# Kernel tuning notes

Measured on AMD Instinct MI355X. Metric: run time of the kernel, lower is better.

The kernel has to match this reference:

```python
import jax, jax.numpy as jnp
import numpy as np


def setup_inputs() -> dict:
    key = jax.random.key(0)
    k1, k2, k3, k4 = jax.random.split(key, 4)
    B, Cin, Cout, H, W = 4, 256, 256, 96, 96
    x = jax.random.normal(k1, (B, Cin, H, W), dtype=jnp.float32)
    offset = jax.random.normal(k2, (B, 18, H, W), dtype=jnp.float32)
    mask = jax.random.uniform(k3, (B, 9, H, W), dtype=jnp.float32)
    weight = jax.random.normal(k4, (Cout, Cin, 3, 3), dtype=jnp.float32) * 0.05
    gamma = jnp.ones((Cout,), dtype=jnp.float32)
    beta = jnp.zeros((Cout,), dtype=jnp.float32)
    return {"x": x, "offset": offset, "mask": mask, "weight": weight, "gamma": gamma, "beta": beta}


def reference(x, offset, mask, weight, gamma, beta):
    # Modulated deformable conv v2 (3x3, stride 1, pad 1, no bias) + GroupNorm(8) + ReLU
    B, C, H, W = x.shape
    O = weight.shape[0]
    K = 9
    xh = jnp.transpose(x, (0, 2, 3, 1))  # [B,H,W,C]
    ky, kx = jnp.meshgrid(jnp.arange(3), jnp.arange(3), indexing="ij")
    ky = ky.reshape(1, K, 1, 1).astype(x.dtype)
    kx = kx.reshape(1, K, 1, 1).astype(x.dtype)
    off = offset.reshape(B, K, 2, H, W)  # (dy, dx) per kernel tap, row-major taps
    gy = jnp.arange(H, dtype=x.dtype).reshape(1, 1, H, 1)
    gx = jnp.arange(W, dtype=x.dtype).reshape(1, 1, 1, W)
    py = gy + ky - 1.0 + off[:, :, 0]  # [B,K,H,W] sampling y
    px = gx + kx - 1.0 + off[:, :, 1]  # [B,K,H,W] sampling x
    y0 = jnp.floor(py)
    x0 = jnp.floor(px)
    wy = py - y0
    wx = px - x0
    y0i = y0.astype(jnp.int32)
    x0i = x0.astype(jnp.int32)
    bidx = jnp.arange(B).reshape(B, 1, 1, 1)

    def gather(yi, xi):
        valid = ((yi >= 0) & (yi < H) & (xi >= 0) & (xi < W)).astype(x.dtype)
        v = xh[bidx, jnp.clip(yi, 0, H - 1), jnp.clip(xi, 0, W - 1)]  # [B,K,H,W,C]
        return v * valid[..., None]

    val = (gather(y0i, x0i) * ((1 - wy) * (1 - wx))[..., None]
           + gather(y0i, x0i + 1) * ((1 - wy) * wx)[..., None]
           + gather(y0i + 1, x0i) * (wy * (1 - wx))[..., None]
           + gather(y0i + 1, x0i + 1) * (wy * wx)[..., None])
    val = val * mask[..., None]  # modulation, [B,K,H,W,C]
    out = jnp.einsum("bkhwc,ock->bohw", val, weight.reshape(O, C, K))
    # GroupNorm with 8 groups, eps=1e-5 (affine)
    G = 8
    og = out.reshape(B, G, O // G, H, W)
    mu = og.mean(axis=(2, 3, 4), keepdims=True)
    var = og.var(axis=(2, 3, 4), keepdims=True)
    og = (og - mu) * jax.lax.rsqrt(var + 1e-5)
    out = og.reshape(B, O, H, W) * gamma.reshape(1, O, 1, 1) + beta.reshape(1, O, 1, 1)
    return jax.nn.relu(out)
```

## Files before the change

kernel.cpp:

```cpp
#include <hip/hip_runtime.h>
#include <hip/hip_bf16.h>
#include <stdint.h>

typedef __attribute__((ext_vector_type(4))) float f32x4;
typedef __attribute__((ext_vector_type(8))) short s16x8;
typedef __attribute__((ext_vector_type(4))) unsigned int u32x4;
typedef unsigned short u16;
typedef unsigned int u32;

#define B_ 4
#define C_ 256
#define O_ 256
#define H_ 96
#define W_ 96
#define HW_ (H_*W_)
#define M_ (B_*HW_)

static __device__ __forceinline__ float asf(u32 u){
    union { u32 u; float f; } x; x.u = u; return x.f;
}
static __device__ __forceinline__ u16 f2bf(float f){
    union { float f; u32 u; } x; x.f = f;
    u32 u = x.u;
    u32 r = (u + 0x7fffu + ((u >> 16) & 1u)) >> 16;
    return (u16)r;
}
static __device__ __forceinline__ u32 blerp_pack(u32 q00, u32 q01, u32 q10, u32 q11,
                                                 float w00, float w01, float w10, float w11)
{
    float f0 = asf(q00 << 16) * w00 + asf(q01 << 16) * w01
             + asf(q10 << 16) * w10 + asf(q11 << 16) * w11;
    float f1 = asf(q00) * w00 + asf(q01) * w01 + asf(q10) * w10 + asf(q11) * w11;
    float2 fp; fp.x = f0; fp.y = f1;
    __hip_bfloat162 hb = __float22bfloat162_rn(fp);
    union { __hip_bfloat162 h; u32 u; } cv; cv.h = hb;
    return cv.u;
}

struct TapCtx {
    float w00, w01, w10, w11;
    const u16 *r00, *r01, *r10, *r11;
};

static __device__ __forceinline__ TapCtx tap_setup(
    int tap, int b, int h, int w, int hw,
    const float* __restrict__ off, const float* __restrict__ msk,
    const u16* __restrict__ xT)
{
    TapCtx t;
    float dy = off[(size_t)(b * 18 + 2 * tap) * HW_ + hw];
    float dx = off[(size_t)(b * 18 + 2 * tap + 1) * HW_ + hw];
    float mk = msk[(size_t)(b * 9 + tap) * HW_ + hw];
    float py = (float)(h + tap / 3 - 1) + dy;
    float px = (float)(w + tap % 3 - 1) + dx;
    float fy = floorf(py), fx = floorf(px);
    float wy = py - fy, wx = px - fx;
    int y0 = (int)fy, x0 = (int)fx;
    int y1 = y0 + 1, x1 = x0 + 1;
    float w00 = (1.f - wy) * (1.f - wx) * mk;
    float w01 = (1.f - wy) * wx * mk;
    float w10 = wy * (1.f - wx) * mk;
    float w11 = wy * wx * mk;
    if (y0 < 0 || y0 >= H_) { w00 = 0.f; w01 = 0.f; }
    if (y1 < 0 || y1 >= H_) { w10 = 0.f; w11 = 0.f; }
    if (x0 < 0 || x0 >= W_) { w00 = 0.f; w10 = 0.f; }
    if (x1 < 0 || x1 >= W_) { w01 = 0.f; w11 = 0.f; }
    int cy0 = min(max(y0, 0), H_ - 1), cy1 = min(max(y1, 0), H_ - 1);
    int cx0 = min(max(x0, 0), W_ - 1), cx1 = min(max(x1, 0), W_ - 1);
    size_t rb = (size_t)b * HW_ * C_;
    t.r00 = xT + rb + ((size_t)cy0 * W_ + cx0) * C_;
    t.r01 = xT + rb + ((size_t)cy0 * W_ + cx1) * C_;
    t.r10 = xT + rb + ((size_t)cy1 * W_ + cx0) * C_;
    t.r11 = xT + rb + ((size_t)cy1 * W_ + cx1) * C_;
    t.w00 = w00; t.w01 = w01; t.w10 = w10; t.w11 = w11;
    return t;
}

__global__ __launch_bounds__(256) void transpose_x(const float* __restrict__ x,
                                                   u16* __restrict__ xT)
{
    __shared__ float t[32][33];
    int tid = threadIdx.x;
    int tx = tid & 31, ty = tid >> 5;
    int bi = blockIdx.x;
    int w0 = (bi % 3) * 32;
    int c0 = ((bi / 3) % 8) * 32;
    int bh = bi / 24;
    int b = bh / H_, h = bh - b * H_;
    #pragma unroll
    for (int r = 0; r < 4; ++r){
        int c = c0 + ty + r * 8;
        t[ty + r * 8][tx] = x[(size_t)(b * C_ + c) * HW_ + h * W_ + w0 + tx];
    }
    __syncthreads();
    #pragma unroll
    for (int r = 0; r < 4; ++r){
        int w = w0 + ty + r * 8;
        xT[((size_t)(b * H_ + h) * W_ + w) * C_ + c0 + tx] = f2bf(t[tx][ty + r * 8]);
    }
}

__global__ __launch_bounds__(256) void pack_w(const float* __restrict__ wt,
                                              u16* __restrict__ w3)
{
    int n = blockIdx.x * 256 + threadIdx.x;
    int o = n / 2304;
    int rem = n - o * 2304;
    int c = rem / 9;
    int tap = rem - c * 9;
    int kidx = tap * 256 + c;
    w3[(size_t)(kidx >> 3) * 2048 + o * 8 + (kidx & 7)] = f2bf(wt[n]);
}

__global__ __launch_bounds__(512, 4) void dcn_main(
    const float* __restrict__ off, const float* __restrict__ msk,
    const u16* __restrict__ xT, const u16* __restrict__ w3,
    float* __restrict__ convOut, float* __restrict__ stats)
{
    __shared__ u16 At[64 * 256];
    int tid = threadIdx.x;
    int lane = tid & 63;
    int wv = tid >> 6;
    int l15 = lane & 15;
    int g = lane >> 4;

    int bid = blockIdx.x;
    int tile = (bid & 7) * 72 + (bid >> 3);
    int b = tile / 144;
    int t = tile - b * 144;
    int ty_ = t / 12, tx_ = t - ty_ * 12;
    int py0 = ty_ * 8, px0 = tx_ * 8;

    f32x4 acc[4][2];
    #pragma unroll
    for (int i = 0; i < 4; ++i)
        #pragma unroll
        for (int q = 0; q < 2; ++q)
            acc[i][q] = (f32x4){0.f, 0.f, 0.f, 0.f};

    int p = tid >> 3;
    int k = tid & 7;
    int h = py0 + (p >> 3);
    int w = px0 + (p & 7);
    int hw = h * W_ + w;

    for (int tap = 0; tap < 9; ++tap){
        __syncthreads();
        TapCtx tp = tap_setup(tap, b, h, w, hw, off, msk, xT);
        #pragma unroll
        for (int i = 0; i < 4; ++i){
            int ck = k + i * 8;
            int c = ck * 8;
            u32x4 q00 = *(const u32x4*)(tp.r00 + c);
            u32x4 q01 = *(const u32x4*)(tp.r01 + c);
            u32x4 q10 = *(const u32x4*)(tp.r10 + c);
            u32x4 q11 = *(const u32x4*)(tp.r11 + c);
            u32x4 outv;
            #pragma unroll
            for (int j = 0; j < 4; ++j)
                outv[j] = blerp_pack(q00[j], q01[j], q10[j], q11[j],
                                     tp.w00, tp.w01, tp.w10, tp.w11);
            u32 boff = (u32)(p * 512) + (u32)((ck ^ (p & 15)) << 4);
            *(u32x4*)((char*)At + boff) = outv;
        }
        __syncthreads();
        __builtin_amdgcn_s_setprio(1);
        #pragma unroll
        for (int step = 0; step < 8; ++step){
            int ck = step * 4 + g;
            s16x8 a[4];
            #pragma unroll
            for (int i = 0; i < 4; ++i){
                int r = i * 16 + l15;
                u32 boff = (u32)(r * 512) + (u32)((ck ^ (r & 15)) << 4);
                a[i] = *(const s16x8*)((const char*)At + boff);
            }
            const u16* wrow = w3 + (size_t)(tap * 32 + step * 4 + g) * 2048
                            + (size_t)(wv * 32 + l15) * 8;
            s16x8 b0 = *(const s16x8*)(wrow);
            s16x8 b1 = *(const s16x8*)(wrow + 128);
            #pragma unroll
            for (int i = 0; i < 4; ++i){
                acc[i][0] = __builtin_amdgcn_mfma_f32_16x16x32_bf16(a[i], b0, acc[i][0], 0, 0, 0);
                acc[i][1] = __builtin_amdgcn_mfma_f32_16x16x32_bf16(a[i], b1, acc[i][1], 0, 0, 0);
            }
        }
        __builtin_amdgcn_s_setprio(0);
    }

    float s0 = 0.f, s20 = 0.f;
    size_t mbase = (size_t)b * HW_;
    #pragma unroll
    for (int i = 0; i < 4; ++i){
        #pragma unroll
        for (int q = 0; q < 2; ++q){
            int oc = wv * 32 + q * 16 + l15;
            #pragma unroll
            for (int j = 0; j < 4; ++j){
                float v = acc[i][q][j];
                int pp = i * 16 + g * 4 + j;
                int mr_hw = (py0 + (pp >> 3)) * W_ + px0 + (pp & 7);
                convOut[(mbase + mr_hw) * 256 + oc] = v;
                s0 += v; s20 += v * v;
            }
        }
    }
    #pragma unroll
    for (int d = 32; d; d >>= 1){
        s0  += __shfl_xor(s0, d, 64);
        s20 += __shfl_xor(s20, d, 64);
    }
    if (lane == 0){
        atomicAdd(&stats[(b * 8 + wv) * 2 + 0], s0);
        atomicAdd(&stats[(b * 8 + wv) * 2 + 1], s20);
    }
}

__global__ __launch_bounds__(256) void gn_final(
    const float* __restrict__ convOut, const float* __restrict__ stats,
    const float* __restrict__ gamma, const float* __restrict__ beta,
    float* __restrict__ out)
{
    __shared__ float t[64][257];
    int tid = threadIdx.x;
    int m0 = blockIdx.x * 64;
    int b = m0 / HW_;
    const f32x4* src = (const f32x4*)(convOut + (size_t)m0 * 256);
    #pragma unroll
    for (int it = 0; it < 16; ++it){
        int idx = it * 256 + tid;
        int r = idx >> 6;
        int c4 = idx & 63;
        f32x4 v = src[(size_t)r * 64 + c4];
        t[r][c4 * 4 + 0] = v[0];
        t[r][c4 * 4 + 1] = v[1];
        t[r][c4 * 4 + 2] = v[2];
        t[r][c4 * 4 + 3] = v[3];
    }
    __syncthreads();
    int lanem = tid & 63;
    int hw = (m0 - b * HW_) + lanem;
    float* dst = out + (size_t)b * O_ * HW_ + hw;
    const float invN = 1.f / 294912.f;
    #pragma unroll 8
    for (int it = 0; it < 64; ++it){
        int o = it * 4 + (tid >> 6);
        int gidx = (b * 8 + (o >> 5)) * 2;
        float sm = stats[gidx + 0];
        float sq = stats[gidx + 1];
        float mu = sm * invN;
        float var = sq * invN - mu * mu;
        float inv = rsqrtf(var + 1e-5f);
        float sc = gamma[o] * inv;
        float sh = beta[o] - mu * sc;
        float v = t[lanem][o];
        dst[(size_t)o * HW_] = fmaxf(v * sc + sh, 0.f);
    }
}

extern "C" void kernel_launch(void* const* d_in, const int* in_sizes, int n_in,
                              void* d_out, int out_size, void* d_ws, size_t ws_size,
                              hipStream_t stream)
{
    const float* x     = (const float*)d_in[0];
    const float* off   = (const float*)d_in[1];
    const float* msk   = (const float*)d_in[2];
    const float* wt    = (const float*)d_in[3];
    const float* gamma = (const float*)d_in[4];
    const float* beta  = (const float*)d_in[5];
    float* out = (float*)d_out;

    char* ws = (char*)d_ws;
    u16*   xT      = (u16*)ws;
    u16*   w3      = (u16*)(ws + 18874368);
    float* convOut = (float*)(ws + 20054016);
    float* stats   = (float*)(ws + 57802752);

    hipMemsetAsync(stats, 0, 256, stream);
    hipLaunchKernelGGL(transpose_x, dim3(9216), dim3(256), 0, stream, x, xT);
    hipLaunchKernelGGL(pack_w,      dim3(2304), dim3(256), 0, stream, wt, w3);
    hipLaunchKernelGGL(dcn_main,    dim3(576),  dim3(512), 0, stream,
                       off, msk, xT, w3, convOut, stats);
    hipLaunchKernelGGL(gn_final,    dim3(576),  dim3(256), 0, stream,
                       convOut, stats, gamma, beta, out);
}
```

Baseline: 183.1 us.

## Double-buffer the sampled tile in LDS and overlap next-tap gather with MFMA

Makes the LDS A-tile double-buffered and software-pipelines the tap loop. The bilinear gather loads for tap+1 are issued before the MFMA steps on the current tap, and the interpolated values are written to the other buffer in two halves between the two MFMA halves. This hides global gather latency behind matrix math and cuts the barriers to one per tap. In exchange it doubles LDS use to 64KB per block, which may limit occupancy under launch_bounds(512,4), and it raises register pressure from the prefetched values.

After: 183.8 us. No clear change (+0.4%).

```diff
diff --git a/kernel.cpp b/kernel.cpp
--- a/kernel.cpp
+++ b/kernel.cpp
@@ -117,7 +117,7 @@
     const u16* __restrict__ xT, const u16* __restrict__ w3,
     float* __restrict__ convOut, float* __restrict__ stats)
 {
-    __shared__ u16 At[64 * 256];
+    __shared__ u16 At[2][64 * 256];
     int tid = threadIdx.x;
     int lane = tid & 63;
     int wv = tid >> 6;
@@ -144,9 +144,8 @@
     int w = px0 + (p & 7);
     int hw = h * W_ + w;
 
-    for (int tap = 0; tap < 9; ++tap){
-        __syncthreads();
-        TapCtx tp = tap_setup(tap, b, h, w, hw, off, msk, xT);
+    {
+        TapCtx tp = tap_setup(0, b, h, w, hw, off, msk, xT);
         #pragma unroll
         for (int i = 0; i < 4; ++i){
             int ck = k + i * 8;
@@ -161,19 +160,40 @@
                 outv[j] = blerp_pack(q00[j], q01[j], q10[j], q11[j],
                                      tp.w00, tp.w01, tp.w10, tp.w11);
             u32 boff = (u32)(p * 512) + (u32)((ck ^ (p & 15)) << 4);
-            *(u32x4*)((char*)At + boff) = outv;
-        }
-        __syncthreads();
+            *(u32x4*)((char*)&At[0][0] + boff) = outv;
+        }
+    }
+    __syncthreads();
+
+    int cur = 0;
+    for (int tap = 0; tap < 9; ++tap){
+        bool pre = (tap < 8);
+        TapCtx tn;
+        u32x4 s00[2], s01[2], s10[2], s11[2];
+        if (pre){
+            tn = tap_setup(tap + 1, b, h, w, hw, off, msk, xT);
+            #pragma unroll
+            for (int i = 0; i < 2; ++i){
+                int c = (k + i * 8) * 8;
+                s00[i] = *(const u32x4*)(tn.r00 + c);
+                s01[i] = *(const u32x4*)(tn.r01 + c);
+                s10[i] = *(const u32x4*)(tn.r10 + c);
+                s11[i] = *(const u32x4*)(tn.r11 + c);
+            }
+        }
+        const char* Ac = (const char*)&At[cur][0];
+        char* An = (char*)&At[cur ^ 1][0];
+
         __builtin_amdgcn_s_setprio(1);
         #pragma unroll
-        for (int step = 0; step < 8; ++step){
+        for (int step = 0; step < 4; ++step){
             int ck = step * 4 + g;
             s16x8 a[4];
             #pragma unroll
             for (int i = 0; i < 4; ++i){
                 int r = i * 16 + l15;
                 u32 boff = (u32)(r * 512) + (u32)((ck ^ (r & 15)) << 4);
-                a[i] = *(const s16x8*)((const char*)At + boff);
+                a[i] = *(const s16x8*)(Ac + boff);
             }
             const u16* wrow = w3 + (size_t)(tap * 32 + step * 4 + g) * 2048
                             + (size_t)(wv * 32 + l15) * 8;
@@ -186,6 +206,67 @@
             }
         }
         __builtin_amdgcn_s_setprio(0);
+
+        if (pre){
+            #pragma unroll
+            for (int i = 0; i < 2; ++i){
+                int ck = k + i * 8;
+                u32x4 outv;
+                #pragma unroll
+                for (int j = 0; j < 4; ++j)
+                    outv[j] = blerp_pack(s00[i][j], s01[i][j], s10[i][j], s11[i][j],
+                                         tn.w00, tn.w01, tn.w10, tn.w11);
+                u32 boff = (u32)(p * 512) + (u32)((ck ^ (p & 15)) << 4);
+                *(u32x4*)(An + boff) = outv;
+            }
+            #pragma unroll
+            for (int i = 0; i < 2; ++i){
+                int c = (k + 16 + i * 8) * 8;
+                s00[i] = *(const u32x4*)(tn.r00 + c);
+                s01[i] = *(const u32x4*)(tn.r01 + c);
+                s10[i] = *(const u32x4*)(tn.r10 + c);
+                s11[i] = *(const u32x4*)(tn.r11 + c);
+            }
+        }
+
+        __builtin_amdgcn_s_setprio(1);
+        #pragma unroll
+        for (int step = 4; step < 8; ++step){
+            int ck = step * 4 + g;
+            s16x8 a[4];
+            #pragma unroll
+            for (int i = 0; i < 4; ++i){
+                int r = i * 16 + l15;
+                u32 boff = (u32)(r * 512) + (u32)((ck ^ (r & 15)) << 4);
+                a[i] = *(const s16x8*)(Ac + boff);
+            }
+            const u16* wrow = w3 + (size_t)(tap * 32 + step * 4 + g) * 2048
+                            + (size_t)(wv * 32 + l15) * 8;
+            s16x8 b0 = *(const s16x8*)(wrow);
+            s16x8 b1 = *(const s16x8*)(wrow + 128);
+            #pragma unroll
+            for (int i = 0; i < 4; ++i){
+                acc[i][0] = __builtin_amdgcn_mfma_f32_16x16x32_bf16(a[i], b0, acc[i][0], 0, 0, 0);
+                acc[i][1] = __builtin_amdgcn_mfma_f32_16x16x32_bf16(a[i], b1, acc[i][1], 0, 0, 0);
+            }
+        }
+        __builtin_amdgcn_s_setprio(0);
+
+        if (pre){
+            #pragma unroll
+            for (int i = 0; i < 2; ++i){
+                int ck = k + 16 + i * 8;
+                u32x4 outv;
+                #pragma unroll
+                for (int j = 0; j < 4; ++j)
+                    outv[j] = blerp_pack(s00[i][j], s01[i][j], s10[i][j], s11[i][j],
+                                         tn.w00, tn.w01, tn.w10, tn.w11);
+                u32 boff = (u32)(p * 512) + (u32)((ck ^ (p & 15)) << 4);
+                *(u32x4*)(An + boff) = outv;
+            }
+        }
+        __syncthreads();
+        cur ^= 1;
     }
 
     float s0 = 0.f, s20 = 0.f;
```

## Stage 16x16 halo of input in LDS and prefetch next tap blend

Applied to the files above, without the earlier changes.

Each block now loads a 16x16 spatial halo (half of the channels at a time) of the transposed input into shared memory and reads bilinear corners from LDS when the sampling point falls inside the halo. Points outside fall back to global loads. The bilinear blend for the next tap is computed while the MFMAs for the current tap run, and offset and mask values are prefetched one tap ahead. The kernel splits channels into two passes and drops the occupancy hint in the launch bounds. LDS use grows to about 80KB and an extra barrier is added per tap.

New measurement: 225.2 us. +23.0%, slower.

```diff
diff --git a/kernel.cpp b/kernel.cpp
--- a/kernel.cpp
+++ b/kernel.cpp
@@ -37,20 +37,16 @@
     return cv.u;
 }
 
-struct TapCtx {
+struct QC {
     float w00, w01, w10, w11;
-    const u16 *r00, *r01, *r10, *r11;
+    int y0, x0, r00, fast;
 };
 
-static __device__ __forceinline__ TapCtx tap_setup(
-    int tap, int b, int h, int w, int hw,
-    const float* __restrict__ off, const float* __restrict__ msk,
-    const u16* __restrict__ xT)
-{
-    TapCtx t;
-    float dy = off[(size_t)(b * 18 + 2 * tap) * HW_ + hw];
-    float dx = off[(size_t)(b * 18 + 2 * tap + 1) * HW_ + hw];
-    float mk = msk[(size_t)(b * 9 + tap) * HW_ + hw];
+static __device__ __forceinline__ QC qc_make(int tap, int h, int w,
+                                             float dy, float dx, float mk,
+                                             int hy0, int hx0)
+{
+    QC t;
     float py = (float)(h + tap / 3 - 1) + dy;
     float px = (float)(w + tap % 3 - 1) + dx;
     float fy = floorf(py), fx = floorf(px);
@@ -65,15 +61,51 @@
     if (y1 < 0 || y1 >= H_) { w10 = 0.f; w11 = 0.f; }
     if (x0 < 0 || x0 >= W_) { w00 = 0.f; w10 = 0.f; }
     if (x1 < 0 || x1 >= W_) { w01 = 0.f; w11 = 0.f; }
-    int cy0 = min(max(y0, 0), H_ - 1), cy1 = min(max(y1, 0), H_ - 1);
-    int cx0 = min(max(x0, 0), W_ - 1), cx1 = min(max(x1, 0), W_ - 1);
-    size_t rb = (size_t)b * HW_ * C_;
-    t.r00 = xT + rb + ((size_t)cy0 * W_ + cx0) * C_;
-    t.r01 = xT + rb + ((size_t)cy0 * W_ + cx1) * C_;
-    t.r10 = xT + rb + ((size_t)cy1 * W_ + cx0) * C_;
-    t.r11 = xT + rb + ((size_t)cy1 * W_ + cx1) * C_;
     t.w00 = w00; t.w01 = w01; t.w10 = w10; t.w11 = w11;
+    t.y0 = y0; t.x0 = x0;
+    t.fast = (y0 >= hy0) && (y0 <= hy0 + 14) && (x0 >= hx0) && (x0 <= hx0 + 14);
+    t.r00 = (y0 - hy0) * 16 + (x0 - hx0);
     return t;
+}
+
+static __device__ __forceinline__ void qblend(const QC& c, int k, int cH,
+                                              const u16* Hl, size_t rbimg,
+                                              const u16* __restrict__ xT,
+                                              u32x4 ov[2])
+{
+    const char* Hb = (const char*)Hl;
+    const u16 *b00 = nullptr, *b01 = nullptr, *b10 = nullptr, *b11 = nullptr;
+    if (!c.fast){
+        int cy0 = min(max(c.y0, 0), H_ - 1), cy1 = min(max(c.y0 + 1, 0), H_ - 1);
+        int cx0 = min(max(c.x0, 0), W_ - 1), cx1 = min(max(c.x0 + 1, 0), W_ - 1);
+        const u16* base = xT + rbimg + cH * 128;
+        b00 = base + ((size_t)cy0 * W_ + cx0) * C_;
+        b01 = base + ((size_t)cy0 * W_ + cx1) * C_;
+        b10 = base + ((size_t)cy1 * W_ + cx0) * C_;
+        b11 = base + ((size_t)cy1 * W_ + cx1) * C_;
+    }
+    int r00 = c.r00, r01 = c.r00 + 1, r10 = c.r00 + 16, r11 = c.r00 + 17;
+    #pragma unroll
+    for (int i = 0; i < 2; ++i){
+        int ck = k + 8 * i;
+        u32x4 q00, q01, q10, q11;
+        if (c.fast){
+            q00 = *(const u32x4*)(Hb + r00 * 256 + ((ck ^ (r00 & 15)) << 4));
+            q01 = *(const u32x4*)(Hb + r01 * 256 + ((ck ^ (r01 & 15)) << 4));
+            q10 = *(const u32x4*)(Hb + r10 * 256 + ((ck ^ (r10 & 15)) << 4));
+            q11 = *(const u32x4*)(Hb + r11 * 256 + ((ck ^ (r11 & 15)) << 4));
+        } else {
+            int cc = ck * 8;
+            q00 = *(const u32x4*)(b00 + cc);
+            q01 = *(const u32x4*)(b01 + cc);
+            q10 = *(const u32x4*)(b10 + cc);
+            q11 = *(const u32x4*)(b11 + cc);
+        }
+        #pragma unroll
+        for (int j = 0; j < 4; ++j)
+            ov[i][j] = blerp_pack(q00[j], q01[j], q10[j], q11[j],
+                                  c.w00, c.w01, c.w10, c.w11);
+    }
 }
 
 __global__ __launch_bounds__(256) void transpose_x(const float* __restrict__ x,
@@ -112,12 +144,14 @@
     w3[(size_t)(kidx >> 3) * 2048 + o * 8 + (kidx & 7)] = f2bf(wt[n]);
 }
 
-__global__ __launch_bounds__(512, 4) void dcn_main(
+__global__ __launch_bounds__(512) void dcn_main(
     const float* __restrict__ off, const float* __restrict__ msk,
     const u16* __restrict__ xT, const u16* __restrict__ w3,
     float* __restrict__ convOut, float* __restrict__ stats)
 {
-    __shared__ u16 At[64 * 256];
+    __shared__ u16 Hl[256 * 128];
+    __shared__ u16 At[64 * 128];
+
     int tid = threadIdx.x;
     int lane = tid & 63;
     int wv = tid >> 6;
@@ -143,49 +177,75 @@
     int h = py0 + (p >> 3);
     int w = px0 + (p & 7);
     int hw = h * W_ + w;
-
-    for (int tap = 0; tap < 9; ++tap){
-        __syncthreads();
-        TapCtx tp = tap_setup(tap, b, h, w, hw, off, msk, xT);
+    size_t offb = (size_t)b * 18 * HW_ + hw;
+    size_t mskb = (size_t)b * 9 * HW_ + hw;
+    int hy0 = py0 - 4, hx0 = px0 - 4;
+    size_t rbimg = (size_t)b * HW_ * C_;
+
+    for (int cH = 0; cH < 2; ++cH){
+        float cdy = off[offb];
+        float cdx = off[offb + HW_];
+        float cmk = msk[mskb];
+        float ndy = off[offb + 2 * HW_];
+        float ndx = off[offb + 3 * HW_];
+        float nmk = msk[mskb + HW_];
         #pragma unroll
-        for (int i = 0; i < 4; ++i){
-            int ck = k + i * 8;
-            int c = ck * 8;
-            u32x4 q00 = *(const u32x4*)(tp.r00 + c);
-            u32x4 q01 = *(const u32x4*)(tp.r01 + c);
-            u32x4 q10 = *(const u32x4*)(tp.r10 + c);
-            u32x4 q11 = *(const u32x4*)(tp.r11 + c);
-            u32x4 outv;
-            #pragma unroll
-            for (int j = 0; j < 4; ++j)
-                outv[j] = blerp_pack(q00[j], q01[j], q10[j], q11[j],
-                                     tp.w00, tp.w01, tp.w10, tp.w11);
-            u32 boff = (u32)(p * 512) + (u32)((ck ^ (p & 15)) << 4);
-            *(u32x4*)((char*)At + boff) = outv;
+        for (int it = 0; it < 8; ++it){
+            int u = it * 512 + tid;
+            int row = u >> 4, ck = u & 15;
+            int gy = min(max(hy0 + (row >> 4), 0), H_ - 1);
+            int gx = min(max(hx0 + (row & 15), 0), W_ - 1);
+            u32x4 v = *(const u32x4*)(xT + rbimg + ((size_t)gy * W_ + gx) * C_
+                                      + cH * 128 + ck * 8);
+            *(u32x4*)((char*)Hl + row * 256 + ((ck ^ (row & 15)) << 4)) = v;
         }
         __syncthreads();
-        __builtin_amdgcn_s_setprio(1);
-        #pragma unroll
-        for (int step = 0; step < 8; ++step){
-            int ck = step * 4 + g;
-            s16x8 a[4];
+
+        QC c = qc_make(0, h, w, cdy, cdx, cmk, hy0, hx0);
+        u32x4 ov[2];
+        qblend(c, k, cH, Hl, rbimg, xT, ov);
+
+        for (int tap = 0; tap < 9; ++tap){
             #pragma unroll
-            for (int i = 0; i < 4; ++i){
-                int r = i * 16 + l15;
-                u32 boff = (u32)(r * 512) + (u32)((ck ^ (r & 15)) << 4);
-                a[i] = *(const s16x8*)((const char*)At + boff);
+            for (int i = 0; i < 2; ++i){
+                int ck = k + 8 * i;
+                *(u32x4*)((char*)At + p * 256 + ((ck ^ (p & 15)) << 4)) = ov[i];
             }
-            const u16* wrow = w3 + (size_t)(tap * 32 + step * 4 + g) * 2048
-                            + (size_t)(wv * 32 + l15) * 8;
-            s16x8 b0 = *(const s16x8*)(wrow);
-            s16x8 b1 = *(const s16x8*)(wrow + 128);
+            __syncthreads();
+
+            if (tap < 8){
+                c = qc_make(tap + 1, h, w, ndy, ndx, nmk, hy0, hx0);
+                qblend(c, k, cH, Hl, rbimg, xT, ov);
+                if (tap < 7){
+                    ndy = off[offb + (size_t)(2 * tap + 4) * HW_];
+                    ndx = off[offb + (size_t)(2 * tap + 5) * HW_];
+                    nmk = msk[mskb + (size_t)(tap + 2) * HW_];
+                }
+            }
+            __builtin_amdgcn_s_setprio(1);
             #pragma unroll
-            for (int i = 0; i < 4; ++i){
-                acc[i][0] = __builtin_amdgcn_mfma_f32_16x16x32_bf16(a[i], b0, acc[i][0], 0, 0, 0);
-                acc[i][1] = __builtin_amdgcn_mfma_f32_16x16x32_bf16(a[i], b1, acc[i][1], 0, 0, 0);
+            for (int s = 0; s < 4; ++s){
+                int ck = s * 4 + g;
+                s16x8 a[4];
+                #pragma unroll
+                for (int i = 0; i < 4; ++i){
+                    int r = i * 16 + l15;
+                    a[i] = *(const s16x8*)((const char*)At + r * 256
+                                           + ((ck ^ (r & 15)) << 4));
+                }
+                const u16* wrow = w3 + (size_t)(tap * 32 + cH * 16 + s * 4 + g) * 2048
+                                + (size_t)(wv * 32 + l15) * 8;
+                s16x8 b0 = *(const s16x8*)(wrow);
+                s16x8 b1 = *(const s16x8*)(wrow + 128);
+                #pragma unroll
+                for (int i = 0; i < 4; ++i){
+                    acc[i][0] = __builtin_amdgcn_mfma_f32_16x16x32_bf16(a[i], b0, acc[i][0], 0, 0, 0);
+                    acc[i][1] = __builtin_amdgcn_mfma_f32_16x16x32_bf16(a[i], b1, acc[i][1], 0, 0, 0);
+                }
             }
+            __builtin_amdgcn_s_setprio(0);
+            __syncthreads();
         }
-        __builtin_amdgcn_s_setprio(0);
     }
 
     float s0 = 0.f, s20 = 0.f;
```

## Double-buffer the sampled A tile and overlap next-tap gather with MFMA

Applied to the files above, without the earlier changes.

Doubles the shared-memory A tile and software-pipelines the tap loop. While the MFMAs for the current tap run, the bilinear gather, interpolation and LDS store for the next tap are interleaved in four chunks. This leaves one barrier per tap and lets gather latency hide behind matrix work. It also switches the gather addresses from 64-bit pointers to 32-bit offsets. The cost is twice the LDS (64KB per block) and more live registers, which may reduce occupancy under the 512x4 launch bound.

Measured after the change: 171.2 us. 6.5% less time.

```diff
diff --git a/kernel.cpp b/kernel.cpp
--- a/kernel.cpp
+++ b/kernel.cpp
@@ -39,13 +39,12 @@
 
 struct TapCtx {
     float w00, w01, w10, w11;
-    const u16 *r00, *r01, *r10, *r11;
+    u32 o00, o01, o10, o11;
 };
 
 static __device__ __forceinline__ TapCtx tap_setup(
     int tap, int b, int h, int w, int hw,
-    const float* __restrict__ off, const float* __restrict__ msk,
-    const u16* __restrict__ xT)
+    const float* __restrict__ off, const float* __restrict__ msk)
 {
     TapCtx t;
     float dy = off[(size_t)(b * 18 + 2 * tap) * HW_ + hw];
@@ -67,11 +66,11 @@
     if (x1 < 0 || x1 >= W_) { w01 = 0.f; w11 = 0.f; }
     int cy0 = min(max(y0, 0), H_ - 1), cy1 = min(max(y1, 0), H_ - 1);
     int cx0 = min(max(x0, 0), W_ - 1), cx1 = min(max(x1, 0), W_ - 1);
-    size_t rb = (size_t)b * HW_ * C_;
-    t.r00 = xT + rb + ((size_t)cy0 * W_ + cx0) * C_;
-    t.r01 = xT + rb + ((size_t)cy0 * W_ + cx1) * C_;
-    t.r10 = xT + rb + ((size_t)cy1 * W_ + cx0) * C_;
-    t.r11 = xT + rb + ((size_t)cy1 * W_ + cx1) * C_;
+    u32 rb = (u32)b * (u32)(HW_ * C_);
+    t.o00 = rb + ((u32)(cy0 * W_ + cx0)) * C_;
+    t.o01 = rb + ((u32)(cy0 * W_ + cx1)) * C_;
+    t.o10 = rb + ((u32)(cy1 * W_ + cx0)) * C_;
+    t.o11 = rb + ((u32)(cy1 * W_ + cx1)) * C_;
     t.w00 = w00; t.w01 = w01; t.w10 = w10; t.w11 = w11;
     return t;
 }
@@ -117,7 +116,7 @@
     const u16* __restrict__ xT, const u16* __restrict__ w3,
     float* __restrict__ convOut, float* __restrict__ stats)
 {
-    __shared__ u16 At[64 * 256];
+    __shared__ u16 At[2][64 * 256];
     int tid = threadIdx.x;
     int lane = tid & 63;
     int wv = tid >> 6;
@@ -144,48 +143,89 @@
     int w = px0 + (p & 7);
     int hw = h * W_ + w;
 
-    for (int tap = 0; tap < 9; ++tap){
-        __syncthreads();
-        TapCtx tp = tap_setup(tap, b, h, w, hw, off, msk, xT);
+    {
+        TapCtx tp = tap_setup(0, b, h, w, hw, off, msk);
         #pragma unroll
         for (int i = 0; i < 4; ++i){
             int ck = k + i * 8;
             int c = ck * 8;
-            u32x4 q00 = *(const u32x4*)(tp.r00 + c);
-            u32x4 q01 = *(const u32x4*)(tp.r01 + c);
-            u32x4 q10 = *(const u32x4*)(tp.r10 + c);
-            u32x4 q11 = *(const u32x4*)(tp.r11 + c);
+            u32x4 q00 = *(const u32x4*)(xT + tp.o00 + c);
+            u32x4 q01 = *(const u32x4*)(xT + tp.o01 + c);
+            u32x4 q10 = *(const u32x4*)(xT + tp.o10 + c);
+            u32x4 q11 = *(const u32x4*)(xT + tp.o11 + c);
             u32x4 outv;
             #pragma unroll
             for (int j = 0; j < 4; ++j)
                 outv[j] = blerp_pack(q00[j], q01[j], q10[j], q11[j],
                                      tp.w00, tp.w01, tp.w10, tp.w11);
             u32 boff = (u32)(p * 512) + (u32)((ck ^ (p & 15)) << 4);
-            *(u32x4*)((char*)At + boff) = outv;
+            *(u32x4*)((char*)&At[0][0] + boff) = outv;
+        }
+    }
+    __syncthreads();
+
+    int cur = 0;
+    for (int tap = 0; tap < 9; ++tap){
+        bool pre = (tap < 8);
+        TapCtx tn;
+        u32x4 s00, s01, s10, s11;
+        if (pre){
+            tn = tap_setup(tap + 1, b, h, w, hw, off, msk);
+            int c = k * 8;
+            s00 = *(const u32x4*)(xT + tn.o00 + c);
+            s01 = *(const u32x4*)(xT + tn.o01 + c);
+            s10 = *(const u32x4*)(xT + tn.o10 + c);
+            s11 = *(const u32x4*)(xT + tn.o11 + c);
+        }
+        const char* Ac = (const char*)&At[cur][0];
+        char* An = (char*)&At[cur ^ 1][0];
+
+        #pragma unroll
+        for (int half = 0; half < 4; ++half){
+            __builtin_amdgcn_s_setprio(1);
+            #pragma unroll
+            for (int s = 0; s < 2; ++s){
+                int step = half * 2 + s;
+                int ck = step * 4 + g;
+                s16x8 a[4];
+                #pragma unroll
+                for (int i = 0; i < 4; ++i){
+                    int r = i * 16 + l15;
+                    u32 boff = (u32)(r * 512) + (u32)((ck ^ (r & 15)) << 4);
+                    a[i] = *(const s16x8*)(Ac + boff);
+                }
+                const u16* wrow = w3 + (size_t)(tap * 32 + step * 4 + g) * 2048
+                                + (size_t)(wv * 32 + l15) * 8;
+                s16x8 b0 = *(const s16x8*)(wrow);
+                s16x8 b1 = *(const s16x8*)(wrow + 128);
+                #pragma unroll
+                for (int i = 0; i < 4; ++i){
+                    acc[i][0] = __builtin_amdgcn_mfma_f32_16x16x32_bf16(a[i], b0, acc[i][0], 0, 0, 0);
+                    acc[i][1] = __builtin_amdgcn_mfma_f32_16x16x32_bf16(a[i], b1, acc[i][1], 0, 0, 0);
+                }
+            }
+            __builtin_amdgcn_s_setprio(0);
+
+            if (pre){
+                int ck = k + half * 8;
+                u32x4 outv;
+                #pragma unroll
+                for (int j = 0; j < 4; ++j)
+                    outv[j] = blerp_pack(s00[j], s01[j], s10[j], s11[j],
+                                         tn.w00, tn.w01, tn.w10, tn.w11);
+                u32 boff = (u32)(p * 512) + (u32)((ck ^ (p & 15)) << 4);
+                *(u32x4*)(An + boff) = outv;
+                if (half < 3){
+                    int c = (k + (half + 1) * 8) * 8;
+                    s00 = *(const u32x4*)(xT + tn.o00 + c);
+                    s01 = *(const u32x4*)(xT + tn.o01 + c);
+                    s10 = *(const u32x4*)(xT + tn.o10 + c);
+                    s11 = *(const u32x4*)(xT + tn.o11 + c);
+                }
+            }
         }
         __syncthreads();
-        __builtin_amdgcn_s_setprio(1);
-        #pragma unroll
-        for (int step = 0; step < 8; ++step){
-            int ck = step * 4 + g;
-            s16x8 a[4];
-            #pragma unroll
-            for (int i = 0; i < 4; ++i){
-                int r = i * 16 + l15;
-                u32 boff = (u32)(r * 512) + (u32)((ck ^ (r & 15)) << 4);
-                a[i] = *(const s16x8*)((const char*)At + boff);
-            }
-            const u16* wrow = w3 + (size_t)(tap * 32 + step * 4 + g) * 2048
-                            + (size_t)(wv * 32 + l15) * 8;
-            s16x8 b0 = *(const s16x8*)(wrow);
-            s16x8 b1 = *(const s16x8*)(wrow + 128);
-            #pragma unroll
-            for (int i = 0; i < 4; ++i){
-                acc[i][0] = __builtin_amdgcn_mfma_f32_16x16x32_bf16(a[i], b0, acc[i][0], 0, 0, 0);
-                acc[i][1] = __builtin_amdgcn_mfma_f32_16x16x32_bf16(a[i], b1, acc[i][1], 0, 0, 0);
-            }
-        }
-        __builtin_amdgcn_s_setprio(0);
+        cur ^= 1;
     }
 
     float s0 = 0.f, s20 = 0.f;
```
